# Optimization experiments

Measured on AMD Instinct MI355X. Metric: run time of the kernel, lower is better.

## Reference

```python
import jax, jax.numpy as jnp
import numpy as np

N_HEADS = 4

def setup_inputs() -> dict:
    key = jax.random.key(0)
    ks = jax.random.split(key, 9)
    B, C, H, W = 4, 256, 64, 64
    nh, hs = N_HEADS, C // N_HEADS
    s = 0.02
    return {
        "x": jax.random.normal(ks[0], (B, C, H, W), jnp.float32),
        "wq": jax.random.normal(ks[1], (C, C), jnp.float32) * s,
        "bq": jax.random.normal(ks[2], (C,), jnp.float32) * s,
        "wk": jax.random.normal(ks[3], (C, C), jnp.float32) * s,
        "bk": jax.random.normal(ks[4], (C,), jnp.float32) * s,
        "wv": jax.random.normal(ks[5], (C, C), jnp.float32) * s,
        "bv": jax.random.normal(ks[6], (C,), jnp.float32) * s,
        "rel_h": jax.random.normal(ks[7], (1, nh, hs, 1, H), jnp.float32),
        "rel_w": jax.random.normal(ks[8], (1, nh, hs, W, 1), jnp.float32),
    }

def reference(x, wq, bq, wk, bk, wv, bv, rel_h, rel_w):
    B, C, H, W = x.shape
    nh = N_HEADS
    hs = C // nh
    S = H * W

    def proj(w, b):
        # 1x1 conv == per-pixel linear over channels -> [B, C, H, W]
        y = jnp.einsum('oc,bchw->bohw', w, x) + b[None, :, None, None]
        # faithful to torch .view: flatten [C,H,W] row-major into [S, nh, hs]
        y = y.reshape(B, S, nh, hs)
        return y.transpose(0, 2, 1, 3)  # [B, nh, S, hs]

    q = proj(wq, bq)
    k = proj(wk, bk)
    v = proj(wv, bv)

    # content scores (NOTE: no 1/sqrt(d) scaling in BoT override)
    attn_content = jnp.einsum('bnqd,bnkd->bnqk', q, k)  # [B, nh, S, S]
    # learned relative position term: broadcast-add then flatten (w,h) order
    pos = (rel_h + rel_w).reshape(1, nh, hs, S)  # [1, nh, hs, S]
    attn_position = jnp.einsum('bnqd,ands->bnqs', q, pos)  # [B, nh, S, S]

    probs = jax.nn.softmax(attn_content + attn_position, axis=-1)
    ctx = jnp.einsum('bnqk,bnkd->bnqd', probs, v)  # [B, nh, S, hs]
    # faithful to torch: transpose(1,2) then view(B, C, width, height)
    out = ctx.transpose(0, 2, 1, 3).reshape(B, C, W, H)
    return out
```

## Files before the change

kernel.cpp:

```cpp
#include <hip/hip_runtime.h>
#include <hip/hip_bf16.h>
#include <stdint.h>
#include <math.h>

typedef __bf16 bf16_t;
typedef __bf16 bf16x8 __attribute__((ext_vector_type(8)));
typedef float  f32x4  __attribute__((ext_vector_type(4)));
typedef float  f32x16 __attribute__((ext_vector_type(16)));
typedef unsigned int u32;

#define S_SZ 4096
#define HS   64
#define OUT_B_STRIDE (256 * 64 * 64)
#define LOG2E 1.4426950408889634f

#define GLOAD_LDS(gsrc, ldst)                                                              \
    __builtin_amdgcn_global_load_lds((__attribute__((address_space(1))) void*)(void*)(gsrc), \
                                     (__attribute__((address_space(3))) void*)(void*)(ldst),  \
                                     16, 0, 0)

static __device__ __forceinline__ u32 pack2(__bf16 a, __bf16 b) {
    return (u32)__builtin_bit_cast(uint16_t, a) | ((u32)__builtin_bit_cast(uint16_t, b) << 16);
}

__global__ __launch_bounds__(256)
void prep_kernel(const float* __restrict__ wq, const float* __restrict__ wk,
                 const float* __restrict__ wv, const float* __restrict__ rel_h,
                 const float* __restrict__ rel_w,
                 bf16_t* __restrict__ Wh, bf16_t* __restrict__ Wl,
                 bf16_t* __restrict__ Rt)
{
    const int blk = blockIdx.x;
    if (blk < 48) {
        const int base = blk * 4096;
        #pragma unroll
        for (int i = 0; i < 16; ++i) {
            const int e = base + i * 256 + threadIdx.x;
            const int o = e >> 8, c = e & 255;
            const float* src = o < 256 ? wq : (o < 512 ? wk : wv);
            float v = src[(size_t)(o & 255) * 256 + c];
            if (o < 256) v *= LOG2E;
            __bf16 h = (__bf16)v;
            Wh[e] = h;
            Wl[e] = (__bf16)(v - (float)h);
        }
    } else {
        const int rb = blk - 48;
        const int n = rb >> 4, h2 = rb & 15;
        __shared__ float rh[4096], rw[4096];
        for (int i = threadIdx.x; i < 4096; i += 256) {
            rh[i] = rel_h[n * 4096 + i];
            rw[i] = rel_w[n * 4096 + i];
        }
        __syncthreads();
        bf16_t* Rp = Rt + ((size_t)n * 4096 + h2 * 256) * 64;
        const int d0 = (threadIdx.x & 7) * 8;
        const int ob = threadIdx.x >> 3;
        #pragma unroll
        for (int i = 0; i < 8; ++i) {
            const int o  = i * 32 + ob;
            const int ih = (o & 3) * 16 + h2;
            const int iw = o >> 2;
            bf16x8 rv;
            #pragma unroll
            for (int dd = 0; dd < 8; ++dd)
                rv[dd] = (bf16_t)(rh[(d0 + dd) * 64 + ih] + rw[(d0 + dd) * 64 + iw]);
            *(bf16x8*)(Rp + (size_t)o * 64 + d0) = rv;
        }
    }
}

__global__ __launch_bounds__(512, 2)
void proj_kernel(const float* __restrict__ x,
                 const bf16_t* __restrict__ Wh, const bf16_t* __restrict__ Wl,
                 const float* __restrict__ bq, const float* __restrict__ bk,
                 const float* __restrict__ bv, const bf16_t* __restrict__ Rt,
                 bf16_t* __restrict__ q_ws, bf16_t* __restrict__ k2_ws,
                 bf16_t* __restrict__ vt2_ws)
{
    const int bx = blockIdx.x;
    const int b  = bx >> 6;
    const int h  = bx & 63;
    const int p0 = h * 64;
    const int n  = h & 3;
    const int h2 = h >> 2;
    const int bn = b * 4 + n;
    const int tid = threadIdx.x;

    __shared__ __align__(16) char SM[98304];

    {
        const int cpair = tid & 127, pg = tid >> 7;
        const int c0 = cpair * 2;
        const float* x0 = x + ((size_t)b * 256 + c0) * 4096 + p0 + pg * 16;
        const int sub = (c0 >> 6) * 128;
        const int u   = (c0 >> 3) & 7;
        const int e2  = (c0 & 7) * 2;
        #pragma unroll
        for (int i4 = 0; i4 < 4; ++i4) {
            f32x4 ra = *(const f32x4*)(x0 + i4 * 4);
            f32x4 rb = *(const f32x4*)(x0 + 4096 + i4 * 4);
            #pragma unroll
            for (int i = 0; i < 4; ++i) {
                const int p = pg * 16 + i4 * 4 + i;
                __bf16 ha = (__bf16)ra[i], hb = (__bf16)rb[i];
                float  la = ra[i] - (float)ha, lb = rb[i] - (float)hb;
                const int off = p * 512 + sub + ((u ^ (p & 7)) * 16) + e2;
                *(u32*)(SM + off)         = pack2(ha, hb);
                *(u32*)(SM + 32768 + off) = pack2((__bf16)la, (__bf16)lb);
            }
        }
    }
    __syncthreads();

    const int wid = tid >> 6, lane = tid & 63, l31 = lane & 31, hi = lane >> 5;

    int obs[3], pjs[3];
    const bf16_t* whp[3];
    const bf16_t* wlp[3];
    #pragma unroll
    for (int j = 0; j < 3; ++j) {
        const int of = (wid * 3 + j) * 32;
        pjs[j] = of >> 8;
        obs[j] = of & 255;
        whp[j] = Wh + (size_t)(of + l31) * 256 + hi * 8;
        wlp[j] = Wl + (size_t)(of + l31) * 256 + hi * 8;
    }

    const char* XHp = SM + l31 * 512;
    const char* XLp = SM + 32768 + l31 * 512;

    f32x16 acc[3][2] = {};

    #pragma unroll
    for (int ks = 0; ks < 16; ++ks) {
        bf16x8 wh[3], wl[3];
        #pragma unroll
        for (int j = 0; j < 3; ++j) {
            wh[j] = *(const bf16x8*)(whp[j] + ks * 16);
            wl[j] = *(const bf16x8*)(wlp[j] + ks * 16);
        }
        const int rb_ = (ks >> 2) * 128 + ((((ks * 2 + hi) & 7) ^ (l31 & 7)) * 16);
        bf16x8 xh[2], xl[2];
        #pragma unroll
        for (int pt = 0; pt < 2; ++pt) {
            xh[pt] = *(const bf16x8*)(XHp + pt * 16384 + rb_);
            xl[pt] = *(const bf16x8*)(XLp + pt * 16384 + rb_);
        }
        #pragma unroll
        for (int j = 0; j < 3; ++j)
            #pragma unroll
            for (int pt = 0; pt < 2; ++pt) {
                acc[j][pt] = __builtin_amdgcn_mfma_f32_32x32x16_bf16(wh[j], xh[pt], acc[j][pt], 0, 0, 0);
                acc[j][pt] = __builtin_amdgcn_mfma_f32_32x32x16_bf16(wh[j], xl[pt], acc[j][pt], 0, 0, 0);
                acc[j][pt] = __builtin_amdgcn_mfma_f32_32x32x16_bf16(wl[j], xh[pt], acc[j][pt], 0, 0, 0);
            }
    }
    __syncthreads();

    #pragma unroll
    for (int j = 0; j < 3; ++j) {
        const float* bp = pjs[j] == 0 ? bq : (pjs[j] == 1 ? bk : bv);
        f32x4 bv4[4];
        #pragma unroll
        for (int g2 = 0; g2 < 4; ++g2) {
            bv4[g2] = *(const f32x4*)(bp + obs[j] + hi * 4 + g2 * 8);
            if (pjs[j] == 0) {
                #pragma unroll
                for (int i = 0; i < 4; ++i) bv4[g2][i] *= LOG2E;
            }
        }
        #pragma unroll
        for (int pt = 0; pt < 2; ++pt) {
            const int d = pt * 32 + l31;
            #pragma unroll
            for (int g2 = 0; g2 < 4; ++g2)
                #pragma unroll
                for (int rr = 0; rr < 4; ++rr) {
                    const int o = obs[j] + rr + 4 * hi + 8 * g2;
                    const float v = acc[j][pt][g2 * 4 + rr] + bv4[g2][rr];
                    if (pjs[j] == 0) {
                        *(bf16_t*)(SM + o * 128 + d * 2) = (bf16_t)v;
                    } else if (pjs[j] == 2) {
                        *(bf16_t*)(SM + 32768 + d * 512 + ((o * 2) ^ ((d & 7) << 4))) = (bf16_t)v;
                    } else {
                        *(bf16_t*)(SM + 65536 + o * 128 + d * 2) = (bf16_t)v;
                    }
                }
        }
    }
    __syncthreads();

    {
        bf16_t* qp = q_ws + (size_t)bn * 4096 * 64;
        #pragma unroll
        for (int i = 0; i < 4; ++i) {
            const int c = i * 512 + tid;
            const int o = c >> 3, d8 = c & 7;
            uint4 v = *(const uint4*)(SM + c * 16);
            *(uint4*)(qp + (size_t)(o * 16 + h2) * 64 + d8 * 8) = v;
        }
        bf16_t* vp = vt2_ws + (size_t)bn * 64 * 4096 + h2 * 256;
        #pragma unroll
        for (int i = 0; i < 4; ++i) {
            const int c = i * 512 + tid;
            const int d = c >> 5, k = c & 31;
            uint4 v = *(const uint4*)(SM + 32768 + d * 512 + ((k * 16) ^ ((d & 7) << 4)));
            *(uint4*)(vp + (size_t)d * 4096 + k * 8) = v;
        }
        const bf16_t* Rp = Rt + ((size_t)n * 4096 + h2 * 256) * 64;
        bf16_t* kp = k2_ws + ((size_t)bn * 4096 + h2 * 256) * 64;
        #pragma unroll
        for (int i = 0; i < 4; ++i) {
            const int c = i * 512 + tid;
            bf16x8 kv = *(const bf16x8*)(SM + 65536 + c * 16);
            bf16x8 rv = *(const bf16x8*)(Rp + c * 8);
            bf16x8 res;
            #pragma unroll
            for (int ii = 0; ii < 8; ++ii)
                res[ii] = (__bf16)((float)kv[ii] + (float)rv[ii]);
            *(bf16x8*)(kp + c * 8) = res;
        }
    }
}

__global__ __launch_bounds__(256, 2)
void attn_kernel(const bf16_t* __restrict__ q_ws, const bf16_t* __restrict__ k_ws,
                 const bf16_t* __restrict__ vt_ws, float* __restrict__ out)
{
    const int tid  = threadIdx.x;
    const int wid  = tid >> 6;
    const int lane = tid & 63;
    const int l31  = lane & 31;
    const int hi   = lane >> 5;

    const int wg  = blockIdx.x;
    const int swz = (wg & 7) * 64 + (wg >> 3);
    const int bn  = swz >> 5;
    const int qb  = swz & 31;
    const int b   = bn >> 2, n = bn & 3;

    __shared__ __align__(16) bf16_t Kt[4][64 * 64];
    __shared__ __align__(16) bf16_t Vt[4][64 * 64];

    const bf16_t* Qb = q_ws  + (size_t)bn * S_SZ * HS;
    const bf16_t* Kb = k_ws  + (size_t)bn * S_SZ * HS;
    const bf16_t* Vb = vt_ws + (size_t)bn * HS * S_SZ;

    const int c0 = wid * 64 + lane;
    const int ra = c0 >> 3, ga = (c0 & 7) ^ (ra & 7);
    const bf16_t* ksrcA = Kb + ra * HS + ga * 8;
    const bf16_t* ksrcB = ksrcA + 32 * HS;
    const bf16_t* vsrcA = Vb + (size_t)ra * S_SZ + ga * 8;
    const bf16_t* vsrcB = vsrcA + (size_t)32 * S_SZ;

#define STAGE(buf, ts)                                                        \
    GLOAD_LDS(ksrcA + (size_t)(ts) * 64 * HS, &Kt[buf][wid * 512]);           \
    GLOAD_LDS(ksrcB + (size_t)(ts) * 64 * HS, &Kt[buf][2048 + wid * 512]);    \
    GLOAD_LDS(vsrcA + (ts) * 64,              &Vt[buf][wid * 512]);           \
    GLOAD_LDS(vsrcB + (ts) * 64,              &Vt[buf][2048 + wid * 512]);

    const int q = qb * 128 + wid * 32 + l31;
    bf16x8 qf[4];
    #pragma unroll
    for (int dk = 0; dk < 4; ++dk)
        qf[dk] = *(const bf16x8*)(Qb + (size_t)q * HS + dk * 16 + hi * 8);

    f32x16 oacc[2];
    f32x16 Z16;
    #pragma unroll
    for (int i = 0; i < 16; ++i) { oacc[0][i] = 0.f; oacc[1][i] = 0.f; Z16[i] = 0.f; }
    float lsum = 0.f;

    const int swzme = (l31 & 7) << 4;

#define QKPAIR(DST, BUF)                                                               \
    { const char* Kb_ = (const char*)&Kt[BUF][0] + l31 * 128;                          \
      __builtin_amdgcn_s_setprio(1);                                                   \
      _Pragma("unroll")                                                                \
      for (int hh = 0; hh < 2; ++hh) {                                                 \
          bf16x8 kf[4];                                                                \
          _Pragma("unroll")                                                            \
          for (int dk = 0; dk < 4; ++dk)                                               \
              kf[dk] = *(const bf16x8*)(Kb_ + hh * 4096 + (((2 * dk + hi) * 16) ^ swzme)); \
          DST[hh] = __builtin_amdgcn_mfma_f32_32x32x16_bf16(kf[0], qf[0], Z16, 0, 0, 0);   \
          _Pragma("unroll")                                                            \
          for (int dk = 1; dk < 4; ++dk)                                               \
              DST[hh] = __builtin_amdgcn_mfma_f32_32x32x16_bf16(kf[dk], qf[dk], DST[hh], 0, 0, 0); \
      }                                                                                \
      __builtin_amdgcn_s_setprio(0); }

#define EXPPV(SRC, VBUF)                                                               \
    { u32 Wd[2][4][2];                                                                 \
      float ps[4] = {0.f, 0.f, 0.f, 0.f};                                              \
      _Pragma("unroll")                                                                \
      for (int hh = 0; hh < 2; ++hh)                                                   \
      _Pragma("unroll")                                                                \
      for (int c = 0; c < 4; ++c)                                                      \
      _Pragma("unroll")                                                                \
      for (int tt = 0; tt < 2; ++tt) {                                                 \
          float pa = __builtin_amdgcn_exp2f(SRC[hh][c * 4 + tt * 2]);                  \
          float pb = __builtin_amdgcn_exp2f(SRC[hh][c * 4 + tt * 2 + 1]);              \
          ps[c] += pa + pb;                                                            \
          u32 w_;                                                                      \
          asm("v_cvt_pk_bf16_f32 %0, %1, %2" : "=v"(w_) : "v"(pa), "v"(pb));           \
          Wd[hh][c][tt] = w_; }                                                        \
      lsum += (ps[0] + ps[1]) + (ps[2] + ps[3]);                                       \
      u32 F[4][4];                                                                     \
      _Pragma("unroll")                                                                \
      for (int hh = 0; hh < 2; ++hh)                                                   \
      _Pragma("unroll")                                                                \
      for (int pr = 0; pr < 2; ++pr)                                                   \
      _Pragma("unroll")                                                                \
      for (int tt = 0; tt < 2; ++tt) {                                                 \
          u32 a_ = Wd[hh][2 * pr][tt], b_ = Wd[hh][2 * pr + 1][tt];                    \
          asm("v_permlane32_swap_b32 %0, %1" : "+v"(a_), "+v"(b_));                    \
          F[2 * hh + pr][tt]     = a_;                                                 \
          F[2 * hh + pr][2 + tt] = b_; }                                               \
      const char* Vb_ = (const char*)&Vt[VBUF][0] + l31 * 128;                         \
      __builtin_amdgcn_s_setprio(1);                                                   \
      _Pragma("unroll")                                                                \
      for (int dh = 0; dh < 2; ++dh)                                                   \
      _Pragma("unroll")                                                                \
      for (int kk = 0; kk < 4; ++kk) {                                                 \
          bf16x8 vf = *(const bf16x8*)(Vb_ + dh * 4096 + (((2 * kk + hi) * 16) ^ swzme)); \
          union { u32 u[4]; bf16x8 v; } pf;                                            \
          pf.u[0] = F[kk][0]; pf.u[1] = F[kk][1]; pf.u[2] = F[kk][2]; pf.u[3] = F[kk][3]; \
          oacc[dh] = __builtin_amdgcn_mfma_f32_32x32x16_bf16(vf, pf.v, oacc[dh], 0, 0, 0); } \
      __builtin_amdgcn_s_setprio(0); }

#define ITER(U, SC, SN)                                                                \
    { asm volatile("s_waitcnt vmcnt(4)" ::: "memory");                                 \
      __builtin_amdgcn_s_barrier();                                                    \
      asm volatile("" ::: "memory");                                                   \
      { const int t_ = tb + (U);                                                       \
        const int ts_ = (t_ + 3 > 63) ? 63 : t_ + 3;                                   \
        STAGE(((U) + 3) & 3, ts_); }                                                   \
      QKPAIR(SN, ((U) + 1) & 3);                                                       \
      EXPPV(SC, (U) & 3); }

    STAGE(0, 0); STAGE(1, 1); STAGE(2, 2);
    asm volatile("s_waitcnt vmcnt(8)" ::: "memory");
    __builtin_amdgcn_s_barrier();
    asm volatile("" ::: "memory");

    f32x16 S0[2], S1[2];
    QKPAIR(S0, 0);

    for (int tb = 0; tb < 64; tb += 4) {
        ITER(0, S0, S1);
        ITER(1, S1, S0);
        ITER(2, S0, S1);
        ITER(3, S1, S0);
    }
#undef ITER
#undef EXPPV
#undef QKPAIR
#undef STAGE

    float lt  = lsum + __shfl_xor(lsum, 32);
    float inv = 1.0f / lt;
    float* outp = out + (size_t)b * OUT_B_STRIDE + (size_t)q * 256 + n * 64;
    #pragma unroll
    for (int dh = 0; dh < 2; ++dh)
        #pragma unroll
        for (int g2 = 0; g2 < 4; ++g2) {
            f32x4 v4;
            #pragma unroll
            for (int r = 0; r < 4; ++r) v4[r] = oacc[dh][g2 * 4 + r] * inv;
            *(f32x4*)(outp + dh * 32 + g2 * 8 + hi * 4) = v4;
        }
}

extern "C" void kernel_launch(void* const* d_in, const int* in_sizes, int n_in,
                              void* d_out, int out_size, void* d_ws, size_t ws_size,
                              hipStream_t stream)
{
    const float* x     = (const float*)d_in[0];
    const float* wq    = (const float*)d_in[1];
    const float* bq    = (const float*)d_in[2];
    const float* wk    = (const float*)d_in[3];
    const float* bk    = (const float*)d_in[4];
    const float* wv    = (const float*)d_in[5];
    const float* bv    = (const float*)d_in[6];
    const float* rel_h = (const float*)d_in[7];
    const float* rel_w = (const float*)d_in[8];
    float* out = (float*)d_out;

    bf16_t* q_ws   = (bf16_t*)d_ws;
    bf16_t* k2_ws  = q_ws  + (size_t)16 * S_SZ * HS;
    bf16_t* vt2_ws = k2_ws + (size_t)16 * S_SZ * HS;

    bf16_t* end = (bf16_t*)d_out + (size_t)out_size * 2;
    bf16_t* Wl  = end - 196608;
    bf16_t* Wh  = Wl - 196608;
    bf16_t* Rt  = Wh - 1048576;

    prep_kernel<<<112, 256, 0, stream>>>(wq, wk, wv, rel_h, rel_w, Wh, Wl, Rt);
    proj_kernel<<<256, 512, 0, stream>>>(x, Wh, Wl, bq, bk, bv, Rt,
                                         q_ws, k2_ws, vt2_ws);
    attn_kernel<<<512, 256, 0, stream>>>(q_ws, k2_ws, vt2_ws, out);
}
```

Baseline: 134.5 us.

## Load attention K/V tiles directly into registers, shrink projection LDS buffer

The attention kernel stops staging K and V tiles through a 4-deep LDS ring filled by global_load_lds with barriers. Each wave now loads its K and V MFMA fragments straight from global memory into registers, double-buffering K tiles in software. The QK and PV steps are merged into one macro, and the skewed S0/S1 score pipelining is removed. Separately, the projection kernel reuses one LDS region for the Q and K outputs in two phases, cutting shared memory from 96 KB to 64 KB. The trade is removing barriers and LDS traffic in exchange for redundant global/L2 loads, since all four waves fetch the same K/V, plus higher register pressure and less latency hiding.

```diff
diff --git a/kernel.cpp b/kernel.cpp
--- a/kernel.cpp
+++ b/kernel.cpp
@@ -13,11 +13,6 @@
 #define HS   64
 #define OUT_B_STRIDE (256 * 64 * 64)
 #define LOG2E 1.4426950408889634f
-
-#define GLOAD_LDS(gsrc, ldst)                                                              \
-    __builtin_amdgcn_global_load_lds((__attribute__((address_space(1))) void*)(void*)(gsrc), \
-                                     (__attribute__((address_space(3))) void*)(void*)(ldst),  \
-                                     16, 0, 0)
 
 static __device__ __forceinline__ u32 pack2(__bf16 a, __bf16 b) {
     return (u32)__builtin_bit_cast(uint16_t, a) | ((u32)__builtin_bit_cast(uint16_t, b) << 16);
@@ -87,7 +82,7 @@
     const int bn = b * 4 + n;
     const int tid = threadIdx.x;
 
-    __shared__ __align__(16) char SM[98304];
+    __shared__ __align__(16) char SM[65536];
 
     {
         const int cpair = tid & 127, pg = tid >> 7;
@@ -158,18 +153,24 @@
     }
     __syncthreads();
 
+    f32x4 bias[3][2][4];
     #pragma unroll
     for (int j = 0; j < 3; ++j) {
         const float* bp = pjs[j] == 0 ? bq : (pjs[j] == 1 ? bk : bv);
-        f32x4 bv4[4];
         #pragma unroll
         for (int g2 = 0; g2 < 4; ++g2) {
-            bv4[g2] = *(const f32x4*)(bp + obs[j] + hi * 4 + g2 * 8);
+            f32x4 v = *(const f32x4*)(bp + obs[j] + hi * 4 + g2 * 8);
             if (pjs[j] == 0) {
                 #pragma unroll
-                for (int i = 0; i < 4; ++i) bv4[g2][i] *= LOG2E;
+                for (int i = 0; i < 4; ++i) v[i] *= LOG2E;
             }
-        }
+            bias[j][0][g2] = v;  bias[j][1][g2] = v;
+        }
+    }
+
+    #pragma unroll
+    for (int j = 0; j < 3; ++j) {
+        if (pjs[j] == 1) continue;
         #pragma unroll
         for (int pt = 0; pt < 2; ++pt) {
             const int d = pt * 32 + l31;
@@ -178,19 +179,16 @@
                 #pragma unroll
                 for (int rr = 0; rr < 4; ++rr) {
                     const int o = obs[j] + rr + 4 * hi + 8 * g2;
-                    const float v = acc[j][pt][g2 * 4 + rr] + bv4[g2][rr];
+                    const float v = acc[j][pt][g2 * 4 + rr] + bias[j][pt][g2][rr];
                     if (pjs[j] == 0) {
                         *(bf16_t*)(SM + o * 128 + d * 2) = (bf16_t)v;
-                    } else if (pjs[j] == 2) {
+                    } else {
                         *(bf16_t*)(SM + 32768 + d * 512 + ((o * 2) ^ ((d & 7) << 4))) = (bf16_t)v;
-                    } else {
-                        *(bf16_t*)(SM + 65536 + o * 128 + d * 2) = (bf16_t)v;
                     }
                 }
         }
     }
     __syncthreads();
-
     {
         bf16_t* qp = q_ws + (size_t)bn * 4096 * 64;
         #pragma unroll
@@ -208,12 +206,33 @@
             uint4 v = *(const uint4*)(SM + 32768 + d * 512 + ((k * 16) ^ ((d & 7) << 4)));
             *(uint4*)(vp + (size_t)d * 4096 + k * 8) = v;
         }
+    }
+    __syncthreads();
+
+    #pragma unroll
+    for (int j = 0; j < 3; ++j) {
+        if (pjs[j] != 1) continue;
+        #pragma unroll
+        for (int pt = 0; pt < 2; ++pt) {
+            const int d = pt * 32 + l31;
+            #pragma unroll
+            for (int g2 = 0; g2 < 4; ++g2)
+                #pragma unroll
+                for (int rr = 0; rr < 4; ++rr) {
+                    const int o = obs[j] + rr + 4 * hi + 8 * g2;
+                    *(bf16_t*)(SM + o * 128 + d * 2) =
+                        (bf16_t)(acc[j][pt][g2 * 4 + rr] + bias[j][pt][g2][rr]);
+                }
+        }
+    }
+    __syncthreads();
+    {
         const bf16_t* Rp = Rt + ((size_t)n * 4096 + h2 * 256) * 64;
         bf16_t* kp = k2_ws + ((size_t)bn * 4096 + h2 * 256) * 64;
         #pragma unroll
         for (int i = 0; i < 4; ++i) {
             const int c = i * 512 + tid;
-            bf16x8 kv = *(const bf16x8*)(SM + 65536 + c * 16);
+            bf16x8 kv = *(const bf16x8*)(SM + c * 16);
             bf16x8 rv = *(const bf16x8*)(Rp + c * 8);
             bf16x8 res;
             #pragma unroll
@@ -240,25 +259,9 @@
     const int qb  = swz & 31;
     const int b   = bn >> 2, n = bn & 3;
 
-    __shared__ __align__(16) bf16_t Kt[4][64 * 64];
-    __shared__ __align__(16) bf16_t Vt[4][64 * 64];
-
-    const bf16_t* Qb = q_ws  + (size_t)bn * S_SZ * HS;
-    const bf16_t* Kb = k_ws  + (size_t)bn * S_SZ * HS;
-    const bf16_t* Vb = vt_ws + (size_t)bn * HS * S_SZ;
-
-    const int c0 = wid * 64 + lane;
-    const int ra = c0 >> 3, ga = (c0 & 7) ^ (ra & 7);
-    const bf16_t* ksrcA = Kb + ra * HS + ga * 8;
-    const bf16_t* ksrcB = ksrcA + 32 * HS;
-    const bf16_t* vsrcA = Vb + (size_t)ra * S_SZ + ga * 8;
-    const bf16_t* vsrcB = vsrcA + (size_t)32 * S_SZ;
-
-#define STAGE(buf, ts)                                                        \
-    GLOAD_LDS(ksrcA + (size_t)(ts) * 64 * HS, &Kt[buf][wid * 512]);           \
-    GLOAD_LDS(ksrcB + (size_t)(ts) * 64 * HS, &Kt[buf][2048 + wid * 512]);    \
-    GLOAD_LDS(vsrcA + (ts) * 64,              &Vt[buf][wid * 512]);           \
-    GLOAD_LDS(vsrcB + (ts) * 64,              &Vt[buf][2048 + wid * 512]);
+    const bf16_t* Qb = q_ws + (size_t)bn * S_SZ * HS;
+    const bf16_t* Kp = k_ws  + (size_t)bn * S_SZ * HS + l31 * HS + hi * 8;
+    const bf16_t* Vp = vt_ws + (size_t)bn * HS * S_SZ + (size_t)l31 * S_SZ + hi * 8;
 
     const int q = qb * 128 + wid * 32 + l31;
     bf16x8 qf[4];
@@ -272,26 +275,34 @@
     for (int i = 0; i < 16; ++i) { oacc[0][i] = 0.f; oacc[1][i] = 0.f; Z16[i] = 0.f; }
     float lsum = 0.f;
 
-    const int swzme = (l31 & 7) << 4;
-
-#define QKPAIR(DST, BUF)                                                               \
-    { const char* Kb_ = (const char*)&Kt[BUF][0] + l31 * 128;                          \
+#define LOADK(KF, T)                                                                   \
+    { const bf16_t* p_ = Kp + (size_t)(T) * (64 * HS);                                 \
+      _Pragma("unroll")                                                                \
+      for (int hh = 0; hh < 2; ++hh)                                                   \
+      _Pragma("unroll")                                                                \
+      for (int dk = 0; dk < 4; ++dk)                                                   \
+          KF[hh][dk] = *(const bf16x8*)(p_ + hh * (32 * HS) + dk * 16); }
+
+#define LOADV(VF, T)                                                                   \
+    { const bf16_t* p_ = Vp + (T) * 64;                                                \
+      _Pragma("unroll")                                                                \
+      for (int dh = 0; dh < 2; ++dh)                                                   \
+      _Pragma("unroll")                                                                \
+      for (int kk = 0; kk < 4; ++kk)                                                   \
+          VF[dh][kk] = *(const bf16x8*)(p_ + (size_t)dh * (32 * S_SZ) + kk * 16); }
+
+#define TILE(KF, VF)                                                                   \
+    { f32x16 sacc[2];                                                                  \
       __builtin_amdgcn_s_setprio(1);                                                   \
       _Pragma("unroll")                                                                \
       for (int hh = 0; hh < 2; ++hh) {                                                 \
-          bf16x8 kf[4];                                                                \
-          _Pragma("unroll")                                                            \
-          for (int dk = 0; dk < 4; ++dk)                                               \
-              kf[dk] = *(const bf16x8*)(Kb_ + hh * 4096 + (((2 * dk + hi) * 16) ^ swzme)); \
-          DST[hh] = __builtin_amdgcn_mfma_f32_32x32x16_bf16(kf[0], qf[0], Z16, 0, 0, 0);   \
+          sacc[hh] = __builtin_amdgcn_mfma_f32_32x32x16_bf16(KF[hh][0], qf[0], Z16, 0, 0, 0); \
           _Pragma("unroll")                                                            \
           for (int dk = 1; dk < 4; ++dk)                                               \
-              DST[hh] = __builtin_amdgcn_mfma_f32_32x32x16_bf16(kf[dk], qf[dk], DST[hh], 0, 0, 0); \
+              sacc[hh] = __builtin_amdgcn_mfma_f32_32x32x16_bf16(KF[hh][dk], qf[dk], sacc[hh], 0, 0, 0); \
       }                                                                                \
-      __builtin_amdgcn_s_setprio(0); }
-
-#define EXPPV(SRC, VBUF)                                                               \
-    { u32 Wd[2][4][2];                                                                 \
+      __builtin_amdgcn_s_setprio(0);                                                   \
+      u32 Wd[2][4][2];                                                                 \
       float ps[4] = {0.f, 0.f, 0.f, 0.f};                                              \
       _Pragma("unroll")                                                                \
       for (int hh = 0; hh < 2; ++hh)                                                   \
@@ -299,8 +310,8 @@
       for (int c = 0; c < 4; ++c)                                                      \
       _Pragma("unroll")                                                                \
       for (int tt = 0; tt < 2; ++tt) {                                                 \
-          float pa = __builtin_amdgcn_exp2f(SRC[hh][c * 4 + tt * 2]);                  \
-          float pb = __builtin_amdgcn_exp2f(SRC[hh][c * 4 + tt * 2 + 1]);              \
+          float pa = __builtin_amdgcn_exp2f(sacc[hh][c * 4 + tt * 2]);                 \
+          float pb = __builtin_amdgcn_exp2f(sacc[hh][c * 4 + tt * 2 + 1]);             \
           ps[c] += pa + pb;                                                            \
           u32 w_;                                                                      \
           asm("v_cvt_pk_bf16_f32 %0, %1, %2" : "=v"(w_) : "v"(pa), "v"(pb));           \
@@ -317,46 +328,30 @@
           asm("v_permlane32_swap_b32 %0, %1" : "+v"(a_), "+v"(b_));                    \
           F[2 * hh + pr][tt]     = a_;                                                 \
           F[2 * hh + pr][2 + tt] = b_; }                                               \
-      const char* Vb_ = (const char*)&Vt[VBUF][0] + l31 * 128;                         \
       __builtin_amdgcn_s_setprio(1);                                                   \
       _Pragma("unroll")                                                                \
       for (int dh = 0; dh < 2; ++dh)                                                   \
       _Pragma("unroll")                                                                \
       for (int kk = 0; kk < 4; ++kk) {                                                 \
-          bf16x8 vf = *(const bf16x8*)(Vb_ + dh * 4096 + (((2 * kk + hi) * 16) ^ swzme)); \
           union { u32 u[4]; bf16x8 v; } pf;                                            \
           pf.u[0] = F[kk][0]; pf.u[1] = F[kk][1]; pf.u[2] = F[kk][2]; pf.u[3] = F[kk][3]; \
-          oacc[dh] = __builtin_amdgcn_mfma_f32_32x32x16_bf16(vf, pf.v, oacc[dh], 0, 0, 0); } \
+          oacc[dh] = __builtin_amdgcn_mfma_f32_32x32x16_bf16(VF[dh][kk], pf.v, oacc[dh], 0, 0, 0); } \
       __builtin_amdgcn_s_setprio(0); }
 
-#define ITER(U, SC, SN)                                                                \
-    { asm volatile("s_waitcnt vmcnt(4)" ::: "memory");                                 \
-      __builtin_amdgcn_s_barrier();                                                    \
-      asm volatile("" ::: "memory");                                                   \
-      { const int t_ = tb + (U);                                                       \
-        const int ts_ = (t_ + 3 > 63) ? 63 : t_ + 3;                                   \
-        STAGE(((U) + 3) & 3, ts_); }                                                   \
-      QKPAIR(SN, ((U) + 1) & 3);                                                       \
-      EXPPV(SC, (U) & 3); }
-
-    STAGE(0, 0); STAGE(1, 1); STAGE(2, 2);
-    asm volatile("s_waitcnt vmcnt(8)" ::: "memory");
-    __builtin_amdgcn_s_barrier();
-    asm volatile("" ::: "memory");
-
-    f32x16 S0[2], S1[2];
-    QKPAIR(S0, 0);
-
-    for (int tb = 0; tb < 64; tb += 4) {
-        ITER(0, S0, S1);
-        ITER(1, S1, S0);
-        ITER(2, S0, S1);
-        ITER(3, S1, S0);
-    }
-#undef ITER
-#undef EXPPV
-#undef QKPAIR
-#undef STAGE
+    bf16x8 kfA[2][4], kfB[2][4], vf[2][4];
+
+    LOADK(kfA, 0);
+    for (int t = 0; t < 64; t += 2) {
+        LOADV(vf, t);
+        LOADK(kfB, t + 1);
+        TILE(kfA, vf);
+        LOADV(vf, t + 1);
+        { const int t2 = (t + 2 < 64) ? t + 2 : 63; LOADK(kfA, t2); }
+        TILE(kfB, vf);
+    }
+#undef TILE
+#undef LOADV
+#undef LOADK
 
     float lt  = lsum + __shfl_xor(lsum, 32);
     float inv = 1.0f / lt;
```

New measurement: 275.3 us. 105% more time.

## Split projection kernel across Q/K/V into separate blocks for more parallelism

Applied to the files above, without the earlier changes.

The projection kernel now launches three times as many blocks, and each block computes only one of the Q, K or V projections for its pixel tile instead of all three. This cuts shared memory per block and the accumulator register count, which allows higher occupancy (launch bounds raised to 4 blocks per CU), and it adds software prefetching of the next weight fragment. In exchange, each block redoes the x load and its hi/lo bf16 split, so x is read and converted three times.

```diff
diff --git a/kernel.cpp b/kernel.cpp
--- a/kernel.cpp
+++ b/kernel.cpp
@@ -70,7 +70,7 @@
     }
 }
 
-__global__ __launch_bounds__(512, 2)
+__global__ __launch_bounds__(512, 4)
 void proj_kernel(const float* __restrict__ x,
                  const bf16_t* __restrict__ Wh, const bf16_t* __restrict__ Wl,
                  const float* __restrict__ bq, const float* __restrict__ bk,
@@ -78,24 +78,25 @@
                  bf16_t* __restrict__ q_ws, bf16_t* __restrict__ k2_ws,
                  bf16_t* __restrict__ vt2_ws)
 {
-    const int bx = blockIdx.x;
-    const int b  = bx >> 6;
-    const int h  = bx & 63;
-    const int p0 = h * 64;
-    const int n  = h & 3;
-    const int h2 = h >> 2;
-    const int bn = b * 4 + n;
+    const int bx  = blockIdx.x;
+    const int sub = bx >> 8;
+    const int b   = (bx >> 6) & 3;
+    const int h   = bx & 63;
+    const int p0  = h * 64;
+    const int n   = h & 3;
+    const int h2  = h >> 2;
+    const int bn  = b * 4 + n;
     const int tid = threadIdx.x;
 
-    __shared__ __align__(16) char SM[98304];
+    __shared__ __align__(16) char SM[65536];
 
     {
         const int cpair = tid & 127, pg = tid >> 7;
         const int c0 = cpair * 2;
         const float* x0 = x + ((size_t)b * 256 + c0) * 4096 + p0 + pg * 16;
-        const int sub = (c0 >> 6) * 128;
-        const int u   = (c0 >> 3) & 7;
-        const int e2  = (c0 & 7) * 2;
+        const int sb = (c0 >> 6) * 128;
+        const int u  = (c0 >> 3) & 7;
+        const int e2 = (c0 & 7) * 2;
         #pragma unroll
         for (int i4 = 0; i4 < 4; ++i4) {
             f32x4 ra = *(const f32x4*)(x0 + i4 * 4);
@@ -105,7 +106,7 @@
                 const int p = pg * 16 + i4 * 4 + i;
                 __bf16 ha = (__bf16)ra[i], hb = (__bf16)rb[i];
                 float  la = ra[i] - (float)ha, lb = rb[i] - (float)hb;
-                const int off = p * 512 + sub + ((u ^ (p & 7)) * 16) + e2;
+                const int off = p * 512 + sb + ((u ^ (p & 7)) * 16) + e2;
                 *(u32*)(SM + off)         = pack2(ha, hb);
                 *(u32*)(SM + 32768 + off) = pack2((__bf16)la, (__bf16)lb);
             }
@@ -115,30 +116,25 @@
 
     const int wid = tid >> 6, lane = tid & 63, l31 = lane & 31, hi = lane >> 5;
 
-    int obs[3], pjs[3];
-    const bf16_t* whp[3];
-    const bf16_t* wlp[3];
-    #pragma unroll
-    for (int j = 0; j < 3; ++j) {
-        const int of = (wid * 3 + j) * 32;
-        pjs[j] = of >> 8;
-        obs[j] = of & 255;
-        whp[j] = Wh + (size_t)(of + l31) * 256 + hi * 8;
-        wlp[j] = Wl + (size_t)(of + l31) * 256 + hi * 8;
-    }
+    const int ob_ = wid * 32;
+    const int of  = sub * 256 + ob_;
+    const bf16_t* whp = Wh + (size_t)(of + l31) * 256 + hi * 8;
+    const bf16_t* wlp = Wl + (size_t)(of + l31) * 256 + hi * 8;
 
     const char* XHp = SM + l31 * 512;
     const char* XLp = SM + 32768 + l31 * 512;
 
-    f32x16 acc[3][2] = {};
+    f32x16 acc[2] = {};
+
+    bf16x8 whC = *(const bf16x8*)(whp);
+    bf16x8 wlC = *(const bf16x8*)(wlp);
+    bf16x8 whN, wlN;
 
     #pragma unroll
     for (int ks = 0; ks < 16; ++ks) {
-        bf16x8 wh[3], wl[3];
-        #pragma unroll
-        for (int j = 0; j < 3; ++j) {
-            wh[j] = *(const bf16x8*)(whp[j] + ks * 16);
-            wl[j] = *(const bf16x8*)(wlp[j] + ks * 16);
+        if (ks < 15) {
+            whN = *(const bf16x8*)(whp + (ks + 1) * 16);
+            wlN = *(const bf16x8*)(wlp + (ks + 1) * 16);
         }
         const int rb_ = (ks >> 2) * 128 + ((((ks * 2 + hi) & 7) ^ (l31 & 7)) * 16);
         bf16x8 xh[2], xl[2];
@@ -148,28 +144,27 @@
             xl[pt] = *(const bf16x8*)(XLp + pt * 16384 + rb_);
         }
         #pragma unroll
-        for (int j = 0; j < 3; ++j)
-            #pragma unroll
-            for (int pt = 0; pt < 2; ++pt) {
-                acc[j][pt] = __builtin_amdgcn_mfma_f32_32x32x16_bf16(wh[j], xh[pt], acc[j][pt], 0, 0, 0);
-                acc[j][pt] = __builtin_amdgcn_mfma_f32_32x32x16_bf16(wh[j], xl[pt], acc[j][pt], 0, 0, 0);
-                acc[j][pt] = __builtin_amdgcn_mfma_f32_32x32x16_bf16(wl[j], xh[pt], acc[j][pt], 0, 0, 0);
-            }
+        for (int pt = 0; pt < 2; ++pt) {
+            acc[pt] = __builtin_amdgcn_mfma_f32_32x32x16_bf16(whC, xh[pt], acc[pt], 0, 0, 0);
+            acc[pt] = __builtin_amdgcn_mfma_f32_32x32x16_bf16(whC, xl[pt], acc[pt], 0, 0, 0);
+            acc[pt] = __builtin_amdgcn_mfma_f32_32x32x16_bf16(wlC, xh[pt], acc[pt], 0, 0, 0);
+        }
+        whC = whN; wlC = wlN;
     }
     __syncthreads();
 
+    const float* bp = sub == 0 ? bq : (sub == 1 ? bk : bv);
+    f32x4 bv4[4];
     #pragma unroll
-    for (int j = 0; j < 3; ++j) {
-        const float* bp = pjs[j] == 0 ? bq : (pjs[j] == 1 ? bk : bv);
-        f32x4 bv4[4];
-        #pragma unroll
-        for (int g2 = 0; g2 < 4; ++g2) {
-            bv4[g2] = *(const f32x4*)(bp + obs[j] + hi * 4 + g2 * 8);
-            if (pjs[j] == 0) {
-                #pragma unroll
-                for (int i = 0; i < 4; ++i) bv4[g2][i] *= LOG2E;
-            }
-        }
+    for (int g2 = 0; g2 < 4; ++g2) {
+        bv4[g2] = *(const f32x4*)(bp + ob_ + hi * 4 + g2 * 8);
+        if (sub == 0) {
+            #pragma unroll
+            for (int i = 0; i < 4; ++i) bv4[g2][i] *= LOG2E;
+        }
+    }
+
+    if (sub != 2) {
         #pragma unroll
         for (int pt = 0; pt < 2; ++pt) {
             const int d = pt * 32 + l31;
@@ -177,21 +172,28 @@
             for (int g2 = 0; g2 < 4; ++g2)
                 #pragma unroll
                 for (int rr = 0; rr < 4; ++rr) {
-                    const int o = obs[j] + rr + 4 * hi + 8 * g2;
-                    const float v = acc[j][pt][g2 * 4 + rr] + bv4[g2][rr];
-                    if (pjs[j] == 0) {
-                        *(bf16_t*)(SM + o * 128 + d * 2) = (bf16_t)v;
-                    } else if (pjs[j] == 2) {
-                        *(bf16_t*)(SM + 32768 + d * 512 + ((o * 2) ^ ((d & 7) << 4))) = (bf16_t)v;
-                    } else {
-                        *(bf16_t*)(SM + 65536 + o * 128 + d * 2) = (bf16_t)v;
-                    }
+                    const int o = ob_ + rr + 4 * hi + 8 * g2;
+                    *(bf16_t*)(SM + o * 128 + d * 2) =
+                        (bf16_t)(acc[pt][g2 * 4 + rr] + bv4[g2][rr]);
                 }
         }
+    } else {
+        #pragma unroll
+        for (int pt = 0; pt < 2; ++pt) {
+            const int d = pt * 32 + l31;
+            #pragma unroll
+            for (int g2 = 0; g2 < 4; ++g2)
+                #pragma unroll
+                for (int rr = 0; rr < 4; ++rr) {
+                    const int o = ob_ + rr + 4 * hi + 8 * g2;
+                    *(bf16_t*)(SM + d * 512 + ((o * 2) ^ ((d & 7) << 4))) =
+                        (bf16_t)(acc[pt][g2 * 4 + rr] + bv4[g2][rr]);
+                }
+        }
     }
     __syncthreads();
 
-    {
+    if (sub == 0) {
         bf16_t* qp = q_ws + (size_t)bn * 4096 * 64;
         #pragma unroll
         for (int i = 0; i < 4; ++i) {
@@ -200,26 +202,28 @@
             uint4 v = *(const uint4*)(SM + c * 16);
             *(uint4*)(qp + (size_t)(o * 16 + h2) * 64 + d8 * 8) = v;
         }
+    } else if (sub == 1) {
+        const bf16_t* Rp = Rt + ((size_t)n * 4096 + h2 * 256) * 64;
+        bf16_t* kp = k2_ws + ((size_t)bn * 4096 + h2 * 256) * 64;
+        #pragma unroll
+        for (int i = 0; i < 4; ++i) {
+            const int c = i * 512 + tid;
+            bf16x8 kv = *(const bf16x8*)(SM + c * 16);
+            bf16x8 rv = *(const bf16x8*)(Rp + c * 8);
+            bf16x8 res;
+            #pragma unroll
+            for (int ii = 0; ii < 8; ++ii)
+                res[ii] = (__bf16)((float)kv[ii] + (float)rv[ii]);
+            *(bf16x8*)(kp + c * 8) = res;
+        }
+    } else {
         bf16_t* vp = vt2_ws + (size_t)bn * 64 * 4096 + h2 * 256;
         #pragma unroll
         for (int i = 0; i < 4; ++i) {
             const int c = i * 512 + tid;
             const int d = c >> 5, k = c & 31;
-            uint4 v = *(const uint4*)(SM + 32768 + d * 512 + ((k * 16) ^ ((d & 7) << 4)));
+            uint4 v = *(const uint4*)(SM + d * 512 + ((k * 16) ^ ((d & 7) << 4)));
             *(uint4*)(vp + (size_t)d * 4096 + k * 8) = v;
-        }
-        const bf16_t* Rp = Rt + ((size_t)n * 4096 + h2 * 256) * 64;
-        bf16_t* kp = k2_ws + ((size_t)bn * 4096 + h2 * 256) * 64;
-        #pragma unroll
-        for (int i = 0; i < 4; ++i) {
-            const int c = i * 512 + tid;
-            bf16x8 kv = *(const bf16x8*)(SM + 65536 + c * 16);
-            bf16x8 rv = *(const bf16x8*)(Rp + c * 8);
-            bf16x8 res;
-            #pragma unroll
-            for (int ii = 0; ii < 8; ++ii)
-                res[ii] = (__bf16)((float)kv[ii] + (float)rv[ii]);
-            *(bf16x8*)(kp + c * 8) = res;
         }
     }
 }
@@ -397,7 +401,7 @@
     bf16_t* Rt  = Wh - 1048576;
 
     prep_kernel<<<112, 256, 0, stream>>>(wq, wk, wv, rel_h, rel_w, Wh, Wl, Rt);
-    proj_kernel<<<256, 512, 0, stream>>>(x, Wh, Wl, bq, bk, bv, Rt,
+    proj_kernel<<<768, 512, 0, stream>>>(x, Wh, Wl, bq, bk, bv, Rt,
                                          q_ws, k2_ws, vt2_ws);
     attn_kernel<<<512, 256, 0, stream>>>(q_ws, k2_ws, vt2_ws, out);
 }
```

After: 129.9 us. 3.4% less time.
